# Kernel tuning notes

Hardware: AMD Instinct MI355X
Metric: run time of the kernel (lower is better)

Reference implementation:

```python
import jax, jax.numpy as jnp
import numpy as np

PATCH = 7
STRIDE = 1
ALPHA = 0.05


def extract_patches(im, p=PATCH, s=STRIDE):
    # im: (b, c, h, w) -> (b, n_patches, c*p*p)
    pat = jax.lax.conv_general_dilated_patches(im, (p, p), (s, s), 'VALID')  # (b, c*p*p, H', W')
    b, d = pat.shape[0], pat.shape[1]
    return pat.reshape(b, d, -1).transpose(0, 2, 1)


def _coherence_l2(xp, yp):
    # xp: (Ni, d) input patches, yp: (Nt, d) target patches, both fp16
    d = xp.shape[-1]
    x2 = jnp.sum(xp * xp, axis=-1)                     # (Ni,)
    y2 = jnp.sum(yp * yp, axis=-1)                     # (Nt,)
    cross = jnp.einsum('td,id->ti', yp, xp)            # (Nt, Ni)
    dist = (y2[:, None] + x2[None, :] - 2.0 * cross) / d
    # normalize each target row by its NN distance (+alpha), then min over targets
    dist = dist / (jnp.min(dist, axis=1, keepdims=True) + jnp.asarray(ALPHA, dist.dtype))
    return jnp.min(dist, axis=0).mean()


def setup_inputs() -> dict:
    key = jax.random.key(0)
    k1, k2 = jax.random.split(key)
    x = jax.random.normal(k1, (2, 3, 96, 96), dtype=jnp.float32)
    y = jax.random.normal(k2, (2, 3, 96, 96), dtype=jnp.float32)
    return {"x": x, "y": y}


def reference(x, y):
    x16 = x.astype(jnp.float16)
    y16 = y.astype(jnp.float16)
    xp = extract_patches(x16)   # (b, N, d)
    yp = extract_patches(y16)   # (b, N, d)
    per_image = jax.vmap(_coherence_l2)(xp, yp)  # (b,)
    return per_image.mean()
```

## Files before the change

### kernel.cpp

```cpp
#include <hip/hip_runtime.h>
#include <hip/hip_fp16.h>

#define IMGS 2
#define OW 90
#define NP 8100
#define HW 96
#define CH_STRIDE 9216
#define IMG_STRIDE 27648
#define KP 192
#define MP 8192
#define ALPHA 0.05f
#define INV_D (1.0f/147.0f)
#define PAD_SENTINEL 60000.0f

typedef _Float16 half8 __attribute__((ext_vector_type(8)));
typedef float floatx4 __attribute__((ext_vector_type(4)));

#define GLD_LDS16(gp, lp)                                                     \
    __builtin_amdgcn_global_load_lds(                                         \
        (const __attribute__((address_space(1))) void*)(gp),                  \
        (__attribute__((address_space(3))) void*)(lp), 16, 0, 0)

#define XP_OFF   0
#define YP_OFF   (XP_OFF + IMGS*MP*KP*2)
#define RMIN_OFF (YP_OFF + IMGS*MP*KP*2)
#define CMIN_OFF (RMIN_OFF + IMGS*MP*4)

__global__ __launch_bounds__(256) void k_build(const float* __restrict__ x,
                                               const float* __restrict__ y,
                                               char* __restrict__ wsb) {
    int tid = threadIdx.x;
    int hwv = tid >> 5;
    int l = tid & 31;
    int grow = blockIdx.x * 8 + hwv;
    int tensor = grow >> 14;
    int img = (grow >> 13) & 1;
    int row = grow & (MP - 1);
    const float* src = (tensor ? y : x) + img * IMG_STRIDE;
    int py = row / OW, px = row - py * OW;
    bool rvalid = row < NP;

    float vals[8];
#pragma unroll
    for (int j = 0; j < 8; j++) {
        int k = l * 8 + j;
        float v = 0.0f;
        if (rvalid && k < 147) {
            int c = k / 49;
            int rm = k - c * 49;
            int dy = rm / 7, dx = rm - dy * 7;
            v = src[c * CH_STRIDE + (py + dy) * HW + px + dx];
        }
        vals[j] = (float)(_Float16)v;
    }
    float ss16 = 0.0f;
#pragma unroll
    for (int j = 0; j < 8; j++) ss16 = fmaf(vals[j], vals[j], ss16);
#pragma unroll
    for (int m = 1; m < 32; m <<= 1) ss16 += __shfl_xor(ss16, m, 32);

    half8 h;
#pragma unroll
    for (int j = 0; j < 8; j++) {
        float f = vals[j];
        if (tensor) f *= -2.0f;
        h[j] = (_Float16)f;
    }
    if (l == 18) {
        if (tensor) {
            h[3] = (_Float16)1.0f;
            h[4] = rvalid ? (_Float16)ss16 : (_Float16)0.0f;
        } else {
            h[3] = rvalid ? (_Float16)ss16 : (_Float16)PAD_SENTINEL;
            h[4] = rvalid ? (_Float16)1.0f : (_Float16)0.0f;
        }
    }
    if (l < 24) {
        _Float16* dst = (_Float16*)(wsb + (tensor ? YP_OFF : XP_OFF)) +
                        ((size_t)img * MP + row) * KP + l * 8;
        *(half8*)dst = h;
    }
    if (tid < 8) {
        int gi = blockIdx.x * 8 + tid;
        if (gi < IMGS * MP)
            ((int*)(wsb + RMIN_OFF))[gi] = 0x7f800000;
        else
            ((int*)(wsb + CMIN_OFF))[gi - IMGS * MP] = 0x7f800000;
    }
}

#define R2OFF 8192

#define STAGE64(mat, buf)                                                      \
    {                                                                          \
        int rb_ = w * 16;                                                      \
        _Pragma("unroll") for (int g_ = 0; g_ < 4; g_++) {                     \
            int r_ = rb_ + g_ * 4 + (lane >> 4);                               \
            int gc_ = (lane & 15) ^ (r_ & 7);                                  \
            GLD_LDS16((mat) + (size_t)r_ * KP + gc_ * 8,                       \
                      (buf) + (rb_ + g_ * 4) * 128);                           \
        }                                                                      \
        int r2_ = rb_ + (lane >> 2);                                           \
        int gc2_ = (lane & 3) ^ ((r2_ >> 1) & 3);                              \
        GLD_LDS16((mat) + (size_t)r2_ * KP + 128 + gc2_ * 8,                   \
                  (buf) + R2OFF + rb_ * 32);                                   \
    }

#define READFRAG(buf, row, ks)                                                 \
    ((ks) < 4 ? *(const half8*)(&(buf)[(row) * 128 +                           \
                                       ((((ks) * 4 + quad) ^ ((row) & 7)) * 8)]) \
              : *(const half8*)(&(buf)[R2OFF + (row) * 32 +                    \
                                       ((quad ^ (((row) >> 1) & 3)) * 8)]))

template <int PASS>
__global__ __launch_bounds__(256, 2) void k_gemm(char* __restrict__ wsb) {
    __shared__ __align__(16) _Float16 Buf[2][10240];
    int tid = threadIdx.x;
    int lane = tid & 63, w = tid >> 6;
    int quad = lane >> 4, col16 = lane & 15;
    int q = blockIdx.x;
    int rtile = blockIdx.y;
    int img = blockIdx.z;

    const _Float16* Res = (const _Float16*)(wsb + (PASS == 1 ? YP_OFF : XP_OFF)) +
                          ((size_t)img * MP + rtile * 128) * KP;
    const _Float16* Str = (const _Float16*)(wsb + (PASS == 1 ? XP_OFF : YP_OFF)) +
                          (size_t)img * MP * KP;

    STAGE64(Res, Buf[0]);
    STAGE64(Res + (size_t)64 * KP, Buf[1]);
    __syncthreads();
    half8 rf[8][5];
#pragma unroll
    for (int i = 0; i < 8; i++) {
        const _Float16* rb = (i < 4) ? Buf[0] : Buf[1];
#pragma unroll
        for (int c = 0; c < 5; c++)
            rf[i][c] = READFRAG(rb, (i & 3) * 16 + col16, c);
    }
    __syncthreads();
    STAGE64(Str + (size_t)(q * 16) * 64 * KP, Buf[0]);

    float mn[8];
#pragma unroll
    for (int i = 0; i < 8; i++) mn[i] = 1e30f;
    const int* RM = (const int*)(wsb + RMIN_OFF) + img * MP;
    int srow = w * 16 + col16;

    for (int s = 0; s < 16; s++) {
        __syncthreads();
        if (s < 15)
            STAGE64(Str + (size_t)(q * 16 + s + 1) * 64 * KP, Buf[(s + 1) & 1]);
        const _Float16* sb = Buf[s & 1];

        _Float16 rp = (_Float16)1.0f;
        bool pad = false;
        if (PASS == 2) {
            int rmb = RM[(q * 16 + s) * 64 + srow];
            pad = (rmb == 0x7f800000);
            float d = __int_as_float(rmb) * INV_D;
            rp = (_Float16)(INV_D / (d + ALPHA));
        }

        floatx4 acc[8];
#pragma unroll
        for (int i = 0; i < 8; i++) acc[i] = (floatx4){0.f, 0.f, 0.f, 0.f};
#pragma unroll
        for (int ks = 0; ks < 5; ks++) {
            half8 sf = READFRAG(sb, srow, ks);
            if (PASS == 2) {
                half8 rpv = {rp, rp, rp, rp, rp, rp, rp, rp};
                sf = sf * rpv;
                if (ks == 4 && pad && quad == 2)
                    sf[4] = (_Float16)PAD_SENTINEL;
            }
#pragma unroll
            for (int i = 0; i < 8; i++)
                acc[i] = __builtin_amdgcn_mfma_f32_16x16x32_f16(
                    sf, rf[i][ks], acc[i], 0, 0, 0);
        }
#pragma unroll
        for (int i = 0; i < 8; i++)
            mn[i] = fminf(mn[i], fminf(fminf(acc[i][0], acc[i][1]),
                                       fminf(acc[i][2], acc[i][3])));
    }

    int* dst = (int*)(wsb + (PASS == 1 ? RMIN_OFF : CMIN_OFF)) + img * MP;
#pragma unroll
    for (int i = 0; i < 8; i++) {
        float best = mn[i];
        best = fminf(best, __shfl_xor(best, 16, 64));
        best = fminf(best, __shfl_xor(best, 32, 64));
        int cg = rtile * 128 + i * 16 + col16;
        if (quad == 0 && cg < NP)
            atomicMin(dst + cg, __float_as_int(best));
    }
}

__global__ __launch_bounds__(256) void k_final(const char* __restrict__ wsb,
                                               float* __restrict__ out) {
    __shared__ float red[256];
    int tid = threadIdx.x;
    const int* cm = (const int*)(wsb + CMIN_OFF);
    float s = 0.0f;
    for (int i = tid; i < NP; i += 256) {
        s += __int_as_float(cm[i]);
        s += __int_as_float(cm[MP + i]);
    }
    red[tid] = s;
    __syncthreads();
    for (int st = 128; st > 0; st >>= 1) {
        if (tid < st) red[tid] += red[tid + st];
        __syncthreads();
    }
    if (tid == 0) out[0] = red[0] * (0.5f / NP);
}

extern "C" void kernel_launch(void* const* d_in, const int* in_sizes, int n_in,
                              void* d_out, int out_size, void* d_ws, size_t ws_size,
                              hipStream_t stream) {
    const float* x = (const float*)d_in[0];
    const float* y = (const float*)d_in[1];
    char* wsb = (char*)d_ws;
    float* out = (float*)d_out;

    k_build<<<4096, 256, 0, stream>>>(x, y, wsb);
    k_gemm<1><<<dim3(8, 64, IMGS), 256, 0, stream>>>(wsb);
    k_gemm<2><<<dim3(8, 64, IMGS), 256, 0, stream>>>(wsb);
    k_final<<<1, 256, 0, stream>>>(wsb, out);
}
```

Before: 157.4 us.

## Remap GEMM warps to 64x32 subtiles, stage row-min in LDS, parallelize final reduction

Each wave of the GEMM kernel now holds fragments for 4 resident row tiles across 2 streamed 16-row slices, where before it held 8 resident tiles and 1 streamed slice. This halves the resident fragment registers so occupancy can rise to 3 blocks per CU. In pass 2 the per-row minima are loaded into LDS once per block with async global-to-LDS loads instead of being read from global memory every step. The final reduction runs across 32 blocks using wave shuffles and an atomic accumulator with a completion counter, which adds atomics and depends on the build kernel zeroing the counters.

```diff
diff --git a/kernel.cpp b/kernel.cpp
--- a/kernel.cpp
+++ b/kernel.cpp
@@ -25,6 +25,8 @@
 #define YP_OFF   (XP_OFF + IMGS*MP*KP*2)
 #define RMIN_OFF (YP_OFF + IMGS*MP*KP*2)
 #define CMIN_OFF (RMIN_OFF + IMGS*MP*4)
+#define ACC_OFF  (CMIN_OFF + IMGS*MP*4)
+#define CNT_OFF  (ACC_OFF + 4)
 
 __global__ __launch_bounds__(256) void k_build(const float* __restrict__ x,
                                                const float* __restrict__ y,
@@ -87,6 +89,10 @@
         else
             ((int*)(wsb + CMIN_OFF))[gi - IMGS * MP] = 0x7f800000;
     }
+    if (blockIdx.x == 0 && tid == 0) {
+        *(float*)(wsb + ACC_OFF) = 0.0f;
+        *(int*)(wsb + CNT_OFF) = 0;
+    }
 }
 
 #define R2OFF 8192
@@ -113,8 +119,9 @@
                                        ((quad ^ (((row) >> 1) & 3)) * 8)]))
 
 template <int PASS>
-__global__ __launch_bounds__(256, 2) void k_gemm(char* __restrict__ wsb) {
+__global__ __launch_bounds__(256, 3) void k_gemm(char* __restrict__ wsb) {
     __shared__ __align__(16) _Float16 Buf[2][10240];
+    __shared__ __align__(16) int RMl[1024];
     int tid = threadIdx.x;
     int lane = tid & 63, w = tid >> 6;
     int quad = lane >> 4, col16 = lane & 15;
@@ -129,23 +136,27 @@
 
     STAGE64(Res, Buf[0]);
     STAGE64(Res + (size_t)64 * KP, Buf[1]);
+    if (PASS == 2 && w == 0) {
+        const char* RMg = wsb + RMIN_OFF + ((size_t)img * MP + q * 1024) * 4;
+#pragma unroll
+        for (int g = 0; g < 4; g++)
+            GLD_LDS16(RMg + g * 1024 + lane * 16, &RMl[g * 256]);
+    }
     __syncthreads();
-    half8 rf[8][5];
-#pragma unroll
-    for (int i = 0; i < 8; i++) {
-        const _Float16* rb = (i < 4) ? Buf[0] : Buf[1];
+    half8 rf[4][5];
+    const _Float16* rb = Buf[w >> 1];
+#pragma unroll
+    for (int i = 0; i < 4; i++)
 #pragma unroll
         for (int c = 0; c < 5; c++)
-            rf[i][c] = READFRAG(rb, (i & 3) * 16 + col16, c);
-    }
+            rf[i][c] = READFRAG(rb, i * 16 + col16, c);
     __syncthreads();
     STAGE64(Str + (size_t)(q * 16) * 64 * KP, Buf[0]);
 
-    float mn[8];
-#pragma unroll
-    for (int i = 0; i < 8; i++) mn[i] = 1e30f;
-    const int* RM = (const int*)(wsb + RMIN_OFF) + img * MP;
-    int srow = w * 16 + col16;
+    float mn[4];
+#pragma unroll
+    for (int i = 0; i < 4; i++) mn[i] = 1e30f;
+    int s0 = (w & 1) * 32;
 
     for (int s = 0; s < 16; s++) {
         __syncthreads();
@@ -153,13 +164,15 @@
             STAGE64(Str + (size_t)(q * 16 + s + 1) * 64 * KP, Buf[(s + 1) & 1]);
         const _Float16* sb = Buf[s & 1];
 
-        _Float16 rp = (_Float16)1.0f;
-        bool pad = false;
+        _Float16 rp0 = (_Float16)1.0f, rp1 = (_Float16)1.0f;
+        bool pad0 = false, pad1 = false;
         if (PASS == 2) {
-            int rmb = RM[(q * 16 + s) * 64 + srow];
-            pad = (rmb == 0x7f800000);
-            float d = __int_as_float(rmb) * INV_D;
-            rp = (_Float16)(INV_D / (d + ALPHA));
+            int b0 = RMl[s * 64 + s0 + col16];
+            int b1 = RMl[s * 64 + s0 + 16 + col16];
+            pad0 = (b0 == 0x7f800000);
+            pad1 = (b1 == 0x7f800000);
+            rp0 = (_Float16)(INV_D / (__int_as_float(b0) * INV_D + ALPHA));
+            rp1 = (_Float16)(INV_D / (__int_as_float(b1) * INV_D + ALPHA));
         }
 
         floatx4 acc[8];
@@ -167,53 +180,72 @@
         for (int i = 0; i < 8; i++) acc[i] = (floatx4){0.f, 0.f, 0.f, 0.f};
 #pragma unroll
         for (int ks = 0; ks < 5; ks++) {
-            half8 sf = READFRAG(sb, srow, ks);
+            half8 sf0 = READFRAG(sb, s0 + col16, ks);
+            half8 sf1 = READFRAG(sb, s0 + 16 + col16, ks);
             if (PASS == 2) {
-                half8 rpv = {rp, rp, rp, rp, rp, rp, rp, rp};
-                sf = sf * rpv;
-                if (ks == 4 && pad && quad == 2)
-                    sf[4] = (_Float16)PAD_SENTINEL;
+                half8 v0 = {rp0, rp0, rp0, rp0, rp0, rp0, rp0, rp0};
+                half8 v1 = {rp1, rp1, rp1, rp1, rp1, rp1, rp1, rp1};
+                sf0 = sf0 * v0;
+                sf1 = sf1 * v1;
+                if (ks == 4 && quad == 2) {
+                    if (pad0) sf0[4] = (_Float16)PAD_SENTINEL;
+                    if (pad1) sf1[4] = (_Float16)PAD_SENTINEL;
+                }
             }
 #pragma unroll
-            for (int i = 0; i < 8; i++)
+            for (int i = 0; i < 4; i++) {
                 acc[i] = __builtin_amdgcn_mfma_f32_16x16x32_f16(
-                    sf, rf[i][ks], acc[i], 0, 0, 0);
-        }
-#pragma unroll
-        for (int i = 0; i < 8; i++)
-            mn[i] = fminf(mn[i], fminf(fminf(acc[i][0], acc[i][1]),
-                                       fminf(acc[i][2], acc[i][3])));
+                    sf0, rf[i][ks], acc[i], 0, 0, 0);
+                acc[4 + i] = __builtin_amdgcn_mfma_f32_16x16x32_f16(
+                    sf1, rf[i][ks], acc[4 + i], 0, 0, 0);
+            }
+        }
+#pragma unroll
+        for (int i = 0; i < 4; i++) {
+            float a = fminf(fminf(acc[i][0], acc[i][1]),
+                            fminf(acc[i][2], acc[i][3]));
+            float b = fminf(fminf(acc[4 + i][0], acc[4 + i][1]),
+                            fminf(acc[4 + i][2], acc[4 + i][3]));
+            mn[i] = fminf(mn[i], fminf(a, b));
+        }
     }
 
     int* dst = (int*)(wsb + (PASS == 1 ? RMIN_OFF : CMIN_OFF)) + img * MP;
 #pragma unroll
-    for (int i = 0; i < 8; i++) {
+    for (int i = 0; i < 4; i++) {
         float best = mn[i];
         best = fminf(best, __shfl_xor(best, 16, 64));
         best = fminf(best, __shfl_xor(best, 32, 64));
-        int cg = rtile * 128 + i * 16 + col16;
+        int cg = rtile * 128 + (w >> 1) * 64 + i * 16 + col16;
         if (quad == 0 && cg < NP)
             atomicMin(dst + cg, __float_as_int(best));
     }
 }
 
-__global__ __launch_bounds__(256) void k_final(const char* __restrict__ wsb,
+__global__ __launch_bounds__(256) void k_final(char* __restrict__ wsb,
                                                float* __restrict__ out) {
-    __shared__ float red[256];
+    __shared__ float red[4];
     int tid = threadIdx.x;
+    int gid = blockIdx.x * 256 + tid;
     const int* cm = (const int*)(wsb + CMIN_OFF);
     float s = 0.0f;
-    for (int i = tid; i < NP; i += 256) {
-        s += __int_as_float(cm[i]);
-        s += __int_as_float(cm[MP + i]);
-    }
-    red[tid] = s;
+    if (gid < NP)
+        s = __int_as_float(cm[gid]) + __int_as_float(cm[MP + gid]);
+#pragma unroll
+    for (int m = 1; m < 64; m <<= 1) s += __shfl_xor(s, m, 64);
+    if ((tid & 63) == 0) red[tid >> 6] = s;
     __syncthreads();
-    for (int st = 128; st > 0; st >>= 1) {
-        if (tid < st) red[tid] += red[tid + st];
-        __syncthreads();
-    }
-    if (tid == 0) out[0] = red[0] * (0.5f / NP);
+    if (tid == 0) {
+        float bs = red[0] + red[1] + red[2] + red[3];
+        float* acc = (float*)(wsb + ACC_OFF);
+        int* cnt = (int*)(wsb + CNT_OFF);
+        atomicAdd(acc, bs);
+        __threadfence();
+        if (atomicAdd(cnt, 1) == 31) {
+            float total = atomicAdd(acc, 0.0f);
+            out[0] = total * (0.5f / NP);
+        }
+    }
 }
 
 extern "C" void kernel_launch(void* const* d_in, const int* in_sizes, int n_in,
@@ -227,5 +259,5 @@
     k_build<<<4096, 256, 0, stream>>>(x, y, wsb);
     k_gemm<1><<<dim3(8, 64, IMGS), 256, 0, stream>>>(wsb);
     k_gemm<2><<<dim3(8, 64, IMGS), 256, 0, stream>>>(wsb);
-    k_final<<<1, 256, 0, stream>>>(wsb, out);
-}
+    k_final<<<32, 256, 0, stream>>>(wsb, out);
+}
```

After: 164.7 us. 4.6% more time.
